# Kernel optimization log

Hardware: AMD Instinct MI355X
Metric: run time of the kernel (lower is better)

## Reference

```python
import jax, jax.numpy as jnp
import numpy as np

C = 1024
H = 64
W = 64


def _conv1x1(x, Wt, b):
    # x: [1, Cin, H, W], Wt: [Cout, Cin] -> [1, Cout, H, W]
    return jnp.einsum('oc,bchw->bohw', Wt, x) + b[None, :, None, None]


def setup_inputs() -> dict:
    key = jax.random.key(0)
    ks = jax.random.split(key, 12)
    sc = 1.0 / np.sqrt(C)
    return {
        'x_f': jax.random.normal(ks[0], (1, C, H, W), jnp.float32),
        'x_m': jax.random.normal(ks[1], (1, C, H, W), jnp.float32),
        'x_l': jax.random.normal(ks[2], (1, C, H, W), jnp.float32),
        'Wq': jax.random.normal(ks[3], (C // 2, C), jnp.float32) * sc,
        'bq': jax.random.normal(ks[4], (C // 2,), jnp.float32) * sc,
        'Wk1': jax.random.normal(ks[5], (C // 2, C), jnp.float32) * sc,
        'bk1': jax.random.normal(ks[6], (C // 2,), jnp.float32) * sc,
        'Wk2': jax.random.normal(ks[7], (C // 2, C), jnp.float32) * sc,
        'bk2': jax.random.normal(ks[8], (C // 2,), jnp.float32) * sc,
        'Wv': jax.random.normal(ks[9], (C, C), jnp.float32) * sc,
        'bv': jax.random.normal(ks[10], (C,), jnp.float32) * sc,
        'gamma': jax.random.normal(ks[11], (1,), jnp.float32),
    }


def reference(x_f, x_m, x_l, Wq, bq, Wk1, bk1, Wk2, bk2, Wv, bv, gamma):
    c = x_f.shape[1]
    h, w = x_f.shape[2], x_f.shape[3]
    # torch .view(1, C, -1) on a [1, C/2, H, W] tensor: row-major reshape to [C, H*W/2]
    q = _conv1x1(x_m, Wq, bq).reshape(c, -1).T      # [HW/2, C]
    kf = _conv1x1(x_f, Wk1, bk1).reshape(c, -1)     # [C, HW/2]
    kl = _conv1x1(x_l, Wk2, bk2).reshape(c, -1)     # [C, HW/2]
    att_f = jax.nn.softmax(kf @ q, axis=-1)         # [C, C]
    att_l = jax.nn.softmax(kl @ q, axis=-1)         # [C, C]
    v = _conv1x1(x_m, Wv, bv).reshape(c, -1)        # [C, HW]
    out = att_f @ v + att_l @ v                     # [C, HW]
    out = out.reshape(1, c, h, w)
    return gamma * out + (x_l + x_f) / 2
```

## Files before the change

kernel.cpp:

```cpp
#include <hip/hip_runtime.h>
#include <math.h>


typedef __attribute__((ext_vector_type(8))) short    bf16x8;
typedef __attribute__((ext_vector_type(4))) float    f32x4;

__device__ __forceinline__ unsigned short f2bf(float x) {
    unsigned u = __float_as_uint(x);
    u += 0x7FFFu + ((u >> 16) & 1u);
    return (unsigned short)(u >> 16);
}
__device__ __forceinline__ float bf2f(unsigned short h) {
    return __uint_as_float(((unsigned)h) << 16);
}
__device__ __forceinline__ void split2(float x, unsigned short& h, unsigned short& l) {
    h = f2bf(x);
    l = f2bf(x - bf2f(h));
}

__device__ __forceinline__ size_t swz(int m, int k, int kpan) {
    return ((size_t)((m >> 4) * kpan + (k >> 5))) * 512
         + (size_t)((((k >> 3) & 3) * 16 + (m & 15)) * 8 + (k & 7));
}

__device__ __forceinline__ void gld16(const unsigned short* g, unsigned short* l) {
    __builtin_amdgcn_global_load_lds(
        (const __attribute__((address_space(1))) unsigned int*)g,
        (__attribute__((address_space(3))) unsigned int*)l,
        16, 0, 0);
}

__device__ __forceinline__ bf16x8 gload16(const unsigned short* p) {
    bf16x8 r;
    asm volatile("global_load_dwordx4 %0, %1, off"
                 : "=v"(r) : "v"(p) : "memory");
    return r;
}

#define RAW_BARRIER() asm volatile("s_barrier" ::: "memory")

template<int N>
__device__ __forceinline__ void vmwait() {
    asm volatile("s_waitcnt vmcnt(%0)" :: "i"(N) : "memory");
}

__global__ __launch_bounds__(256) void weights_split_k(
    const float* __restrict__ Wq, const float* __restrict__ Wk1,
    const float* __restrict__ Wk2, const float* __restrict__ Wv,
    unsigned short* __restrict__ Wqh, unsigned short* __restrict__ Wql,
    unsigned short* __restrict__ Wk1h, unsigned short* __restrict__ Wk1l,
    unsigned short* __restrict__ Wk2h, unsigned short* __restrict__ Wk2l,
    unsigned short* __restrict__ Wvh, unsigned short* __restrict__ Wvl)
{
    const int gi = blockIdx.x;
    const float* src; unsigned short *H, *L; int base;
    if (gi < 512)       { src = Wq;  H = Wqh;  L = Wql;  base = gi; }
    else if (gi < 1024) { src = Wk1; H = Wk1h; L = Wk1l; base = gi - 512; }
    else if (gi < 1536) { src = Wk2; H = Wk2h; L = Wk2l; base = gi - 1024; }
    else                { src = Wv;  H = Wvh;  L = Wvl;  base = gi - 1536; }
    const size_t i = (size_t)base * 1024 + threadIdx.x * 4;
    const int m = (int)(i >> 10);
    const int k = (int)(i & 1023);
    const float4 v = *(const float4*)(src + i);
    ushort4 h, l;
    split2(v.x, h.x, l.x); split2(v.y, h.y, l.y);
    split2(v.z, h.z, l.z); split2(v.w, h.w, l.w);
    const size_t o = swz(m, k, 32);
    *(ushort4*)(H + o) = h;
    *(ushort4*)(L + o) = l;
}

__global__ __launch_bounds__(256) void transpose3_k(
    const float* __restrict__ x0, const float* __restrict__ x1,
    const float* __restrict__ x2,
    unsigned short* __restrict__ t0h, unsigned short* __restrict__ t0l,
    unsigned short* __restrict__ t1h, unsigned short* __restrict__ t1l,
    unsigned short* __restrict__ t2h, unsigned short* __restrict__ t2l)
{
    const float* X; unsigned short *Th, *Tl;
    if (blockIdx.z == 0)      { X = x0; Th = t0h; Tl = t0l; }
    else if (blockIdx.z == 1) { X = x1; Th = t1h; Tl = t1l; }
    else                      { X = x2; Th = t2h; Tl = t2l; }

    __shared__ float t[32 * 33];
    const int tid = threadIdx.x;
    const int c0 = blockIdx.y * 32;
    const int p0 = blockIdx.x * 32;

    const int cl = tid >> 3;
    const int p4 = (tid & 7) * 4;
    const float4 v = *(const float4*)(X + (size_t)(c0 + cl) * 4096 + p0 + p4);
    t[(p4 + 0) * 33 + cl] = v.x;
    t[(p4 + 1) * 33 + cl] = v.y;
    t[(p4 + 2) * 33 + cl] = v.z;
    t[(p4 + 3) * 33 + cl] = v.w;
    __syncthreads();

    const int pl = tid >> 3;
    const int c4 = (tid & 7) * 4;
    ushort4 h, l;
    split2(t[pl * 33 + c4 + 0], h.x, l.x);
    split2(t[pl * 33 + c4 + 1], h.y, l.y);
    split2(t[pl * 33 + c4 + 2], h.z, l.z);
    split2(t[pl * 33 + c4 + 3], h.w, l.w);
    const size_t o = (size_t)(p0 + pl) * 1024 + c0 + c4;
    *(ushort4*)(Th + o) = h;
    *(ushort4*)(Tl + o) = l;
}

template<int TERMS, int NJ>
__device__ __forceinline__ void gemm_core(
    const unsigned short* __restrict__ Ah, const unsigned short* __restrict__ Al,
    const unsigned short* __restrict__ Bh, const unsigned short* __restrict__ Bl,
    int ldkB, int kpanA, int kbeg, int kend, int m0, int n0,
    unsigned short* Bs_h, unsigned short* Bs_l,
    f32x4 (&acc)[4][NJ])
{
    const int tid  = threadIdx.x;
    const int lane = tid & 63;
    const int wv   = tid >> 6;
    const int wm   = (wv >> 1) * 64;
    const int wn   = (wv & 1) * (16 * NJ);
    const int lr   = lane & 15;
    const int quad = lane >> 4;
    const int BUFE = 1024 * NJ;
    constexpr int AOPS = (TERMS == 3 ? 8 : 4);

    const unsigned short* gsrc = (wv < 2) ? Bh : Bl;
    unsigned short* ldst = (wv < 2) ? Bs_h : Bs_l;
    const int tt0  = (wv & 1) * NJ;
    const int lrow = lane >> 2;
    const int gseg = ((lane & 3) - ((lane >> 3) & 3)) & 3;
    const size_t bstep = (size_t)16 * (size_t)ldkB;
    const unsigned short* gp0 =
        gsrc + (size_t)(n0 + tt0 * 16 + lrow) * ldkB + kbeg + gseg * 8;

    const int pk0 = kbeg >> 5;
    const size_t astr  = (size_t)kpanA * 512;
    const size_t abase = (size_t)((m0 + wm) >> 4) * astr + (size_t)pk0 * 512
                       + (size_t)lane * 8;
    const unsigned short* ap0 = Ah + abase;
    const unsigned short* al0 = (TERMS == 3) ? (Al + abase) : nullptr;

    const int rdseg = (quad + (lr >> 1)) & 3;

    const int nsteps = (kend - kbeg) >> 5;

#pragma unroll
    for (int u = 0; u < NJ; ++u)
        gld16(gp0 + (size_t)u * bstep, ldst + 0 * BUFE + (tt0 + u) * 512);

    bf16x8 cah[4], cal[4], nah[4], nal[4];
#pragma unroll
    for (int i = 0; i < 4; ++i) {
        cah[i] = gload16(ap0 + (size_t)i * astr);
        if (TERMS == 3) cal[i] = gload16(al0 + (size_t)i * astr);
    }
#pragma unroll
    for (int u = 0; u < NJ; ++u)
        gld16(gp0 + (size_t)u * bstep + 32, ldst + 1 * BUFE + (tt0 + u) * 512);

    vmwait<AOPS + NJ>();
    RAW_BARRIER();

    int br = 0;
    int bw = 2;

#define GSTEP(S, CH, CL, NH, NL)                                              \
    {                                                                         \
        const bool hasA = (S) + 1 < nsteps;                                   \
        const bool hasD = (S) + 2 < nsteps;                                   \
        if (hasA) {                                                           \
            const size_t aoff = (size_t)((S) + 1) * 512;                      \
            _Pragma("unroll")                                                 \
            for (int i = 0; i < 4; ++i) {                                     \
                NH[i] = gload16(ap0 + (size_t)i * astr + aoff);               \
                if (TERMS == 3)                                               \
                    NL[i] = gload16(al0 + (size_t)i * astr + aoff);           \
            }                                                                 \
        }                                                                     \
        if (hasD) {                                                           \
            const size_t goff = (size_t)((S) + 2) * 32;                       \
            unsigned short* dst = ldst + bw * BUFE;                           \
            _Pragma("unroll")                                                 \
            for (int u = 0; u < NJ; ++u)                                      \
                gld16(gp0 + (size_t)u * bstep + goff, dst + (tt0 + u) * 512); \
        }                                                                     \
        if (hasA && hasD) vmwait<AOPS + NJ>();                                \
        else if (hasA)    vmwait<AOPS>();                                     \
        else              vmwait<0>();                                        \
        __builtin_amdgcn_sched_barrier(0);                                    \
        const int rbase = br * BUFE + (wn + lr) * 32 + rdseg * 8;             \
        _Pragma("unroll")                                                     \
        for (int j = 0; j < NJ; ++j) {                                        \
            const bf16x8 bh = *(const bf16x8*)(Bs_h + rbase + j * 512);       \
            const bf16x8 bl = *(const bf16x8*)(Bs_l + rbase + j * 512);       \
            _Pragma("unroll")                                                 \
            for (int i = 0; i < 4; ++i) {                                     \
                acc[i][j] = __builtin_amdgcn_mfma_f32_16x16x32_bf16(          \
                    CH[i], bh, acc[i][j], 0, 0, 0);                           \
                acc[i][j] = __builtin_amdgcn_mfma_f32_16x16x32_bf16(          \
                    CH[i], bl, acc[i][j], 0, 0, 0);                           \
                if (TERMS == 3)                                               \
                    acc[i][j] = __builtin_amdgcn_mfma_f32_16x16x32_bf16(      \
                        CL[i], bh, acc[i][j], 0, 0, 0);                       \
            }                                                                 \
        }                                                                     \
        RAW_BARRIER();                                                        \
        br = (br == 2) ? 0 : br + 1;                                          \
        bw = (bw == 2) ? 0 : bw + 1;                                          \
    }

    for (int s = 0; s < nsteps; s += 2) {
        GSTEP(s,     cah, cal, nah, nal);
        GSTEP(s + 1, nah, nal, cah, cal);
    }
#undef GSTEP
}

#define GEMM_PROLOGUE(NJ_)                                              \
    __shared__ __align__(16) unsigned short Bs_h[3 * 1024 * (NJ_)];     \
    __shared__ __align__(16) unsigned short Bs_l[3 * 1024 * (NJ_)];     \
    f32x4 acc[4][(NJ_)];                                                \
    _Pragma("unroll") for (int i = 0; i < 4; ++i)                       \
    _Pragma("unroll") for (int j = 0; j < (NJ_); ++j)                   \
    _Pragma("unroll") for (int r = 0; r < 4; ++r) acc[i][j][r] = 0.f;   \
    const int lane = threadIdx.x & 63;                                  \
    const int wv   = threadIdx.x >> 6;                                  \
    const int wm   = (wv >> 1) * 64;                                    \
    const int wn   = (wv & 1) * (16 * (NJ_));                           \
    const int lr   = lane & 15;                                         \
    const int quad = lane >> 4;                                         \
    (void)lane; (void)wv; (void)wm; (void)wn;

__global__ __launch_bounds__(256, 2) void conv_all_k(
    const unsigned short* __restrict__ Wqh, const unsigned short* __restrict__ Wql,
    const unsigned short* __restrict__ Wk1h, const unsigned short* __restrict__ Wk1l,
    const unsigned short* __restrict__ Wk2h, const unsigned short* __restrict__ Wk2l,
    const unsigned short* __restrict__ Wvh, const unsigned short* __restrict__ Wvl,
    const unsigned short* __restrict__ xmTh, const unsigned short* __restrict__ xmTl,
    const unsigned short* __restrict__ xfTh, const unsigned short* __restrict__ xfTl,
    const unsigned short* __restrict__ xlTh, const unsigned short* __restrict__ xlTl,
    const float* __restrict__ bq, const float* __restrict__ bk1,
    const float* __restrict__ bk2, const float* __restrict__ bv,
    unsigned short* __restrict__ Qh, unsigned short* __restrict__ Ql,
    unsigned short* __restrict__ Kfh, unsigned short* __restrict__ Kfl,
    unsigned short* __restrict__ Klh, unsigned short* __restrict__ Kll,
    unsigned short* __restrict__ VTh, unsigned short* __restrict__ VTl)
{
    GEMM_PROLOGUE(4);
    const int lid = blockIdx.y * 32 + blockIdx.x;
    const int wg  = (lid & 7) * 80 + (lid >> 3);
    const int mt  = wg >> 5;
    const int n0  = (wg & 31) * 128;

    const unsigned short *Ah, *Al, *Bh, *Bl;
    const float* bias;
    unsigned short *Ch = nullptr, *Cl = nullptr;
    int mloc, mode;
    if (mt < 4) {
        Ah = Wqh;  Al = Wql;  Bh = xmTh; Bl = xmTl; bias = bq;
        Ch = Qh;   Cl = Ql;   mloc = mt * 128;        mode = 0;
    } else if (mt < 8) {
        Ah = Wk1h; Al = Wk1l; Bh = xfTh; Bl = xfTl; bias = bk1;
        Ch = Kfh;  Cl = Kfl;  mloc = (mt - 4) * 128;  mode = 1;
    } else if (mt < 12) {
        Ah = Wk2h; Al = Wk2l; Bh = xlTh; Bl = xlTl; bias = bk2;
        Ch = Klh;  Cl = Kll;  mloc = (mt - 8) * 128;  mode = 1;
    } else {
        Ah = Wvh;  Al = Wvl;  Bh = xmTh; Bl = xmTl; bias = bv;
        mloc = (mt - 12) * 128;                       mode = 2;
    }

    gemm_core<3, 4>(Ah, Al, Bh, Bl, 1024, 32, 0, 1024, mloc, n0, Bs_h, Bs_l, acc);

    if (mode == 2) {
        __syncthreads();
        unsigned short (*Sh)[136] = (unsigned short (*)[136])Bs_h;
        unsigned short (*Sl)[136] = (unsigned short (*)[136])Bs_l;
        const int myhalf = (wv & 1);
#pragma unroll
        for (int sb = 0; sb < 4; ++sb) {
            if ((sb >> 1) == myhalf) {
                const int jbase = (sb & 1) * 2;
#pragma unroll
                for (int jj = 0; jj < 2; ++jj) {
                    const int j = jbase + jj;
                    const int prow = jj * 16 + lr;
#pragma unroll
                    for (int i = 0; i < 4; ++i) {
#pragma unroll
                        for (int r = 0; r < 4; ++r) {
                            const int c = wm + i * 16 + quad * 4 + r;
                            const float v = acc[i][j][r] + bias[mloc + c];
                            unsigned short h, l;
                            split2(v, h, l);
                            Sh[prow][c] = h;
                            Sl[prow][c] = l;
                        }
                    }
                }
            }
            __syncthreads();
            {
                const int pl2 = threadIdx.x >> 3;
                const int c0  = (threadIdx.x & 7) * 16;
                const size_t ob = (size_t)(n0 + sb * 32 + pl2) * 1024 + mloc + c0;
                *(bf16x8*)(VTh + ob)     = *(const bf16x8*)&Sh[pl2][c0];
                *(bf16x8*)(VTh + ob + 8) = *(const bf16x8*)&Sh[pl2][c0 + 8];
                *(bf16x8*)(VTl + ob)     = *(const bf16x8*)&Sl[pl2][c0];
                *(bf16x8*)(VTl + ob + 8) = *(const bf16x8*)&Sl[pl2][c0 + 8];
            }
            __syncthreads();
        }
        return;
    }

#pragma unroll
    for (int i = 0; i < 4; ++i) {
        const int mb = mloc + wm + i * 16 + quad * 4;
#pragma unroll
        for (int j = 0; j < 4; ++j) {
            const int nn = n0 + wn + j * 16 + lr;
#pragma unroll
            for (int r = 0; r < 4; ++r) {
                const float v = acc[i][j][r] + bias[mb + r];
                if (mode == 0) {
                    unsigned short h, l;
                    split2(v, h, l);
                    const size_t idx = (size_t)(mb + r) * 4096 + nn;
                    Ch[idx] = h;
                    Cl[idx] = l;
                } else {
                    const int m2 = ((mb + r) << 1) | (nn >> 11);
                    const int k2 = nn & 2047;
                    const size_t o = swz(m2, k2, 64);
                    unsigned short h, l;
                    split2(v, h, l);
                    Ch[o] = h;
                    Cl[o] = l;
                }
            }
        }
    }
}

__global__ __launch_bounds__(256, 2) void logits_fused_k(
    const unsigned short* __restrict__ Kfh, const unsigned short* __restrict__ Kfl,
    const unsigned short* __restrict__ Klh, const unsigned short* __restrict__ Kll,
    const unsigned short* __restrict__ Qh, const unsigned short* __restrict__ Ql,
    float* __restrict__ Sfp, float* __restrict__ Slp)
{
    GEMM_PROLOGUE(4);
    const int lid = (blockIdx.z * 8 + blockIdx.y) * 8 + blockIdx.x;
    const int wg  = (lid & 7) * 64 + (lid >> 3);
    const int bx  = wg & 7;
    const int by  = (wg >> 3) & 7;
    const int bz  = wg >> 6;

    const int which = bz >> 2;
    const int slice = bz & 3;
    const unsigned short* Ah = which ? Klh : Kfh;
    const unsigned short* Al = which ? Kll : Kfl;
    float* out = (which ? Slp : Sfp) + (size_t)slice * 1024 * 1024;
    const int m0 = by * 128;
    const int n0 = bx * 128;

    gemm_core<3, 4>(Ah, Al, Qh, Ql, 2048, 64, slice * 512, slice * 512 + 512,
                    m0, n0, Bs_h, Bs_l, acc);

#pragma unroll
    for (int i = 0; i < 4; ++i) {
        const int mb = m0 + wm + i * 16 + quad * 4;
#pragma unroll
        for (int j = 0; j < 4; ++j) {
            const int nn = n0 + wn + j * 16 + lr;
#pragma unroll
            for (int r = 0; r < 4; ++r)
                out[(size_t)(mb + r) * 1024 + nn] = acc[i][j][r];
        }
    }
}

__global__ __launch_bounds__(256, 2) void gemm_final_k(
    const unsigned short* __restrict__ Amh,
    const unsigned short* __restrict__ VTh, const unsigned short* __restrict__ VTl,
    float* __restrict__ out,
    const float* __restrict__ xf, const float* __restrict__ xl,
    const float* __restrict__ gamma)
{
    GEMM_PROLOGUE(4);
    const int m0 = blockIdx.y * 128;
    const int n0 = blockIdx.x * 128;

    gemm_core<2, 4>(Amh, nullptr, VTh, VTl, 1024, 32, 0, 1024, m0, n0,
                    Bs_h, Bs_l, acc);

    const float g = gamma[0];
#pragma unroll
    for (int i = 0; i < 4; ++i) {
        const int mb = m0 + wm + i * 16 + quad * 4;
#pragma unroll
        for (int j = 0; j < 4; ++j) {
            const int nn = n0 + wn + j * 16 + lr;
#pragma unroll
            for (int r = 0; r < 4; ++r) {
                const size_t idx = (size_t)(mb + r) * 4096 + nn;
                out[idx] = g * acc[i][j][r] + 0.5f * (xf[idx] + xl[idx]);
            }
        }
    }
}

__global__ __launch_bounds__(256) void softmax_add4_k(
    const float* __restrict__ Sfp, const float* __restrict__ Slp,
    unsigned short* __restrict__ Ah)
{
    const int row = blockIdx.x;
    const int tid = threadIdx.x;
    __shared__ float red[8];
    const size_t base = (size_t)row * 1024 + tid * 4;
    const size_t SL = (size_t)1024 * 1024;

    float4 vf = *(const float4*)(Sfp + base);
    float4 vl = *(const float4*)(Slp + base);
#pragma unroll
    for (int s = 1; s < 4; ++s) {
        const float4 a = *(const float4*)(Sfp + s * SL + base);
        const float4 b = *(const float4*)(Slp + s * SL + base);
        vf.x += a.x; vf.y += a.y; vf.z += a.z; vf.w += a.w;
        vl.x += b.x; vl.y += b.y; vl.z += b.z; vl.w += b.w;
    }

    float mf = fmaxf(fmaxf(vf.x, vf.y), fmaxf(vf.z, vf.w));
    float ml = fmaxf(fmaxf(vl.x, vl.y), fmaxf(vl.z, vl.w));
#pragma unroll
    for (int off = 32; off; off >>= 1) {
        mf = fmaxf(mf, __shfl_down(mf, off, 64));
        ml = fmaxf(ml, __shfl_down(ml, off, 64));
    }
    const int wave = tid >> 6;
    if ((tid & 63) == 0) { red[wave] = mf; red[4 + wave] = ml; }
    __syncthreads();
    mf = fmaxf(fmaxf(red[0], red[1]), fmaxf(red[2], red[3]));
    ml = fmaxf(fmaxf(red[4], red[5]), fmaxf(red[6], red[7]));
    __syncthreads();

    const float4 ef = make_float4(expf(vf.x - mf), expf(vf.y - mf),
                                  expf(vf.z - mf), expf(vf.w - mf));
    const float4 el = make_float4(expf(vl.x - ml), expf(vl.y - ml),
                                  expf(vl.z - ml), expf(vl.w - ml));
    float sf = ef.x + ef.y + ef.z + ef.w;
    float sl = el.x + el.y + el.z + el.w;
#pragma unroll
    for (int off = 32; off; off >>= 1) {
        sf += __shfl_down(sf, off, 64);
        sl += __shfl_down(sl, off, 64);
    }
    if ((tid & 63) == 0) { red[wave] = sf; red[4 + wave] = sl; }
    __syncthreads();
    sf = red[0] + red[1] + red[2] + red[3];
    sl = red[4] + red[5] + red[6] + red[7];

    const float rf = 1.f / sf, rl = 1.f / sl;
    ushort4 h;
    h.x = f2bf(ef.x * rf + el.x * rl);
    h.y = f2bf(ef.y * rf + el.y * rl);
    h.z = f2bf(ef.z * rf + el.z * rl);
    h.w = f2bf(ef.w * rf + el.w * rl);
    const size_t o = swz(row, tid * 4, 32);
    *(ushort4*)(Ah + o) = h;
}

__global__ void noop_k(float* p) { if (threadIdx.x == 1024) p[0] = 0.f; }

extern "C" void kernel_launch(void* const* d_in, const int* in_sizes, int n_in,
                              void* d_out, int out_size, void* d_ws, size_t ws_size,
                              hipStream_t stream) {
    (void)in_sizes; (void)n_in; (void)out_size;
    const float* xf  = (const float*)d_in[0];
    const float* xm  = (const float*)d_in[1];
    const float* xl  = (const float*)d_in[2];
    const float* Wq  = (const float*)d_in[3];
    const float* bq  = (const float*)d_in[4];
    const float* Wk1 = (const float*)d_in[5];
    const float* bk1 = (const float*)d_in[6];
    const float* Wk2 = (const float*)d_in[7];
    const float* bk2 = (const float*)d_in[8];
    const float* Wv  = (const float*)d_in[9];
    const float* bv  = (const float*)d_in[10];
    const float* gamma = (const float*)d_in[11];
    float* out = (float*)d_out;

    const size_t MB = 1024 * 1024;
    if (ws_size < 98 * MB) {
        noop_k<<<dim3(1), dim3(64), 0, stream>>>((float*)d_ws);
        return;
    }

    char* p = (char*)d_ws;
    unsigned short* xmT_h = (unsigned short*)(p + 0 * MB);
    unsigned short* xmT_l = (unsigned short*)(p + 8 * MB);
    unsigned short* xfT_h = (unsigned short*)(p + 16 * MB);
    unsigned short* xfT_l = (unsigned short*)(p + 24 * MB);
    unsigned short* xlT_h = (unsigned short*)(p + 32 * MB);
    unsigned short* xlT_l = (unsigned short*)(p + 40 * MB);
    unsigned short* Wq_h  = (unsigned short*)(p + 48 * MB);
    unsigned short* Wq_l  = (unsigned short*)(p + 49 * MB);
    unsigned short* Wk1_h = (unsigned short*)(p + 50 * MB);
    unsigned short* Wk1_l = (unsigned short*)(p + 51 * MB);
    unsigned short* Wk2_h = (unsigned short*)(p + 52 * MB);
    unsigned short* Wk2_l = (unsigned short*)(p + 53 * MB);
    unsigned short* Wv_h  = (unsigned short*)(p + 54 * MB);
    unsigned short* Wv_l  = (unsigned short*)(p + 56 * MB);
    unsigned short* Q_h   = (unsigned short*)(p + 58 * MB);
    unsigned short* Q_l   = (unsigned short*)(p + 62 * MB);
    unsigned short* Kf_h  = (unsigned short*)(p + 66 * MB);
    unsigned short* Kf_l  = (unsigned short*)(p + 70 * MB);
    unsigned short* Kl_h  = (unsigned short*)(p + 74 * MB);
    unsigned short* Kl_l  = (unsigned short*)(p + 78 * MB);
    unsigned short* VT_h  = (unsigned short*)(p + 82 * MB);
    unsigned short* VT_l  = (unsigned short*)(p + 90 * MB);
    float*          Sfp  = (float*)(p + 16 * MB);
    float*          Slp  = (float*)(p + 32 * MB);
    unsigned short* Am_h = (unsigned short*)(p + 74 * MB);

    const dim3 blk(256);
    transpose3_k<<<dim3(128, 32, 3), blk, 0, stream>>>(
        xm, xf, xl, xmT_h, xmT_l, xfT_h, xfT_l, xlT_h, xlT_l);
    weights_split_k<<<dim3(2560), blk, 0, stream>>>(
        Wq, Wk1, Wk2, Wv, Wq_h, Wq_l, Wk1_h, Wk1_l, Wk2_h, Wk2_l, Wv_h, Wv_l);
    conv_all_k<<<dim3(32, 20), blk, 0, stream>>>(
        Wq_h, Wq_l, Wk1_h, Wk1_l, Wk2_h, Wk2_l, Wv_h, Wv_l,
        xmT_h, xmT_l, xfT_h, xfT_l, xlT_h, xlT_l,
        bq, bk1, bk2, bv,
        Q_h, Q_l, Kf_h, Kf_l, Kl_h, Kl_l, VT_h, VT_l);
    logits_fused_k<<<dim3(8, 8, 8), blk, 0, stream>>>(
        Kf_h, Kf_l, Kl_h, Kl_l, Q_h, Q_l, Sfp, Slp);
    softmax_add4_k<<<dim3(1024), blk, 0, stream>>>(Sfp, Slp, Am_h);
    gemm_final_k<<<dim3(32, 8), blk, 0, stream>>>(
        Am_h, VT_h, VT_l, out, xf, xl, gamma);
}
```

Baseline: 268.7 us.

## Simplify GEMM pipeline to double buffering and raise occupancy to four blocks

Replaces the triple-buffered LDS ring and the register-prefetched A fragments with a simpler double-buffered loop. A fragments are now loaded at the top of each step rather than one step ahead. LDS per block drops from three to two buffers, and launch bounds move from 2 to 4 blocks per CU, so more waves can hide latency. In exchange, A-load latency is no longer overlapped with the previous step's MFMAs, each step adds an extra barrier, and the tighter register budget may cause spills.

```diff
diff --git a/kernel.cpp b/kernel.cpp
--- a/kernel.cpp
+++ b/kernel.cpp
@@ -124,7 +124,6 @@
     const int lr   = lane & 15;
     const int quad = lane >> 4;
     const int BUFE = 1024 * NJ;
-    constexpr int AOPS = (TERMS == 3 ? 8 : 4);
 
     const unsigned short* gsrc = (wv < 2) ? Bh : Bl;
     unsigned short* ldst = (wv < 2) ? Bs_h : Bs_l;
@@ -139,8 +138,8 @@
     const size_t astr  = (size_t)kpanA * 512;
     const size_t abase = (size_t)((m0 + wm) >> 4) * astr + (size_t)pk0 * 512
                        + (size_t)lane * 8;
-    const unsigned short* ap0 = Ah + abase;
-    const unsigned short* al0 = (TERMS == 3) ? (Al + abase) : nullptr;
+    const unsigned short* ap = Ah + abase;
+    const unsigned short* al = (TERMS == 3) ? (Al + abase) : nullptr;
 
     const int rdseg = (quad + (lr >> 1)) & 3;
 
@@ -150,77 +149,52 @@
     for (int u = 0; u < NJ; ++u)
         gld16(gp0 + (size_t)u * bstep, ldst + 0 * BUFE + (tt0 + u) * 512);
 
-    bf16x8 cah[4], cal[4], nah[4], nal[4];
-#pragma unroll
-    for (int i = 0; i < 4; ++i) {
-        cah[i] = gload16(ap0 + (size_t)i * astr);
-        if (TERMS == 3) cal[i] = gload16(al0 + (size_t)i * astr);
-    }
-#pragma unroll
-    for (int u = 0; u < NJ; ++u)
-        gld16(gp0 + (size_t)u * bstep + 32, ldst + 1 * BUFE + (tt0 + u) * 512);
-
-    vmwait<AOPS + NJ>();
-    RAW_BARRIER();
-
-    int br = 0;
-    int bw = 2;
-
-#define GSTEP(S, CH, CL, NH, NL)                                              \
-    {                                                                         \
-        const bool hasA = (S) + 1 < nsteps;                                   \
-        const bool hasD = (S) + 2 < nsteps;                                   \
-        if (hasA) {                                                           \
-            const size_t aoff = (size_t)((S) + 1) * 512;                      \
-            _Pragma("unroll")                                                 \
-            for (int i = 0; i < 4; ++i) {                                     \
-                NH[i] = gload16(ap0 + (size_t)i * astr + aoff);               \
-                if (TERMS == 3)                                               \
-                    NL[i] = gload16(al0 + (size_t)i * astr + aoff);           \
-            }                                                                 \
-        }                                                                     \
-        if (hasD) {                                                           \
-            const size_t goff = (size_t)((S) + 2) * 32;                       \
-            unsigned short* dst = ldst + bw * BUFE;                           \
-            _Pragma("unroll")                                                 \
-            for (int u = 0; u < NJ; ++u)                                      \
-                gld16(gp0 + (size_t)u * bstep + goff, dst + (tt0 + u) * 512); \
-        }                                                                     \
-        if (hasA && hasD) vmwait<AOPS + NJ>();                                \
-        else if (hasA)    vmwait<AOPS>();                                     \
-        else              vmwait<0>();                                        \
-        __builtin_amdgcn_sched_barrier(0);                                    \
-        const int rbase = br * BUFE + (wn + lr) * 32 + rdseg * 8;             \
-        _Pragma("unroll")                                                     \
-        for (int j = 0; j < NJ; ++j) {                                        \
-            const bf16x8 bh = *(const bf16x8*)(Bs_h + rbase + j * 512);       \
-            const bf16x8 bl = *(const bf16x8*)(Bs_l + rbase + j * 512);       \
-            _Pragma("unroll")                                                 \
-            for (int i = 0; i < 4; ++i) {                                     \
-                acc[i][j] = __builtin_amdgcn_mfma_f32_16x16x32_bf16(          \
-                    CH[i], bh, acc[i][j], 0, 0, 0);                           \
-                acc[i][j] = __builtin_amdgcn_mfma_f32_16x16x32_bf16(          \
-                    CH[i], bl, acc[i][j], 0, 0, 0);                           \
-                if (TERMS == 3)                                               \
-                    acc[i][j] = __builtin_amdgcn_mfma_f32_16x16x32_bf16(      \
-                        CL[i], bh, acc[i][j], 0, 0, 0);                       \
-            }                                                                 \
-        }                                                                     \
-        RAW_BARRIER();                                                        \
-        br = (br == 2) ? 0 : br + 1;                                          \
-        bw = (bw == 2) ? 0 : bw + 1;                                          \
-    }
-
-    for (int s = 0; s < nsteps; s += 2) {
-        GSTEP(s,     cah, cal, nah, nal);
-        GSTEP(s + 1, nah, nal, cah, cal);
-    }
-#undef GSTEP
+    bf16x8 cah[4], cal[4];
+    size_t goff = 32;
+
+    for (int s = 0; s < nsteps; ++s) {
+        RAW_BARRIER();
+#pragma unroll
+        for (int i = 0; i < 4; ++i) {
+            cah[i] = gload16(ap + (size_t)i * astr);
+            if (TERMS == 3) cal[i] = gload16(al + (size_t)i * astr);
+        }
+        ap += 512;
+        if (TERMS == 3) al += 512;
+        if (s + 1 < nsteps) {
+            unsigned short* dst = ldst + ((s + 1) & 1) * BUFE;
+#pragma unroll
+            for (int u = 0; u < NJ; ++u)
+                gld16(gp0 + (size_t)u * bstep + goff, dst + (tt0 + u) * 512);
+            goff += 32;
+            vmwait<NJ>();
+        } else {
+            vmwait<0>();
+        }
+        RAW_BARRIER();
+        __builtin_amdgcn_sched_barrier(0);
+        const int rbase = (s & 1) * BUFE + (wn + lr) * 32 + rdseg * 8;
+#pragma unroll
+        for (int j = 0; j < NJ; ++j) {
+            const bf16x8 bh = *(const bf16x8*)(Bs_h + rbase + j * 512);
+            const bf16x8 bl = *(const bf16x8*)(Bs_l + rbase + j * 512);
+#pragma unroll
+            for (int i = 0; i < 4; ++i) {
+                acc[i][j] = __builtin_amdgcn_mfma_f32_16x16x32_bf16(
+                    cah[i], bh, acc[i][j], 0, 0, 0);
+                acc[i][j] = __builtin_amdgcn_mfma_f32_16x16x32_bf16(
+                    cah[i], bl, acc[i][j], 0, 0, 0);
+                if (TERMS == 3)
+                    acc[i][j] = __builtin_amdgcn_mfma_f32_16x16x32_bf16(
+                        cal[i], bh, acc[i][j], 0, 0, 0);
+            }
+        }
+    }
 }
 
 #define GEMM_PROLOGUE(NJ_)                                              \
-    __shared__ __align__(16) unsigned short Bs_h[3 * 1024 * (NJ_)];     \
-    __shared__ __align__(16) unsigned short Bs_l[3 * 1024 * (NJ_)];     \
+    __shared__ __align__(16) unsigned short Bs_h[2 * 1024 * (NJ_)];     \
+    __shared__ __align__(16) unsigned short Bs_l[2 * 1024 * (NJ_)];     \
     f32x4 acc[4][(NJ_)];                                                \
     _Pragma("unroll") for (int i = 0; i < 4; ++i)                       \
     _Pragma("unroll") for (int j = 0; j < (NJ_); ++j)                   \
@@ -233,7 +207,7 @@
     const int quad = lane >> 4;                                         \
     (void)lane; (void)wv; (void)wm; (void)wn;
 
-__global__ __launch_bounds__(256, 2) void conv_all_k(
+__global__ __launch_bounds__(256, 4) void conv_all_k(
     const unsigned short* __restrict__ Wqh, const unsigned short* __restrict__ Wql,
     const unsigned short* __restrict__ Wk1h, const unsigned short* __restrict__ Wk1l,
     const unsigned short* __restrict__ Wk2h, const unsigned short* __restrict__ Wk2l,
@@ -345,7 +319,7 @@
     }
 }
 
-__global__ __launch_bounds__(256, 2) void logits_fused_k(
+__global__ __launch_bounds__(256, 4) void logits_fused_k(
     const unsigned short* __restrict__ Kfh, const unsigned short* __restrict__ Kfl,
     const unsigned short* __restrict__ Klh, const unsigned short* __restrict__ Kll,
     const unsigned short* __restrict__ Qh, const unsigned short* __restrict__ Ql,
@@ -382,7 +356,7 @@
     }
 }
 
-__global__ __launch_bounds__(256, 2) void gemm_final_k(
+__global__ __launch_bounds__(256, 4) void gemm_final_k(
     const unsigned short* __restrict__ Amh,
     const unsigned short* __restrict__ VTh, const unsigned short* __restrict__ VTl,
     float* __restrict__ out,
```

Result: no change. 272.3 us (+1.3%).
